# Performance work log

Measured on AMD Instinct MI355X. Metric: run time of the kernel, lower is better.

## Reference

```python
import jax, jax.numpy as jnp
import numpy as np

B, T, N, D, H = 16, 128, 64, 256, 512

def _xavier(key, shape):
    fan_in, fan_out = shape[0], shape[1]
    limit = float(np.sqrt(6.0 / (fan_in + fan_out)))
    return jax.random.uniform(key, shape, jnp.float32, -limit, limit)

def setup_inputs() -> dict:
    key = jax.random.key(0)
    ks = jax.random.split(key, 12)
    inp = {
        'x1': jax.random.normal(ks[0], (B, T, N, D), jnp.float32),
        'x2': jax.random.normal(ks[1], (B, T, N, D), jnp.float32),
        'Wq1': _xavier(ks[2], (D, H)),
        'Wk1': _xavier(ks[3], (D, H)),
        'Wv1': _xavier(ks[4], (D, H)),
        'Wq2': _xavier(ks[5], (D, H)),
        'Wk2': _xavier(ks[6], (D, H)),
        'Wv2': _xavier(ks[7], (D, H)),
        'W1': _xavier(ks[8], (2 * H, H)),
        'b1': jnp.zeros((H,), jnp.float32),
        'W2': _xavier(ks[9], (H, H)),
        'b2': jnp.zeros((H,), jnp.float32),
    }
    return inp

def reference(x1, x2, Wq1, Wk1, Wv1, Wq2, Wk2, Wv2, W1, b1, W2, b2):
    scale = x1.shape[-1] ** (-0.5)  # scales by in_dim, as in the original
    q1 = jnp.einsum('btnd,dh->btnh', x1, Wq1) * scale
    k1 = jnp.einsum('btnd,dh->btnh', x1, Wk1)
    v1 = jnp.einsum('btnd,dh->btnh', x1, Wv1)
    q2 = jnp.einsum('btnd,dh->btnh', x2, Wq2) * scale
    k2 = jnp.einsum('btnd,dh->btnh', x2, Wk2)
    v2 = jnp.einsum('btnd,dh->btnh', x2, Wv2)
    # cross attention 1: q1 attends over k2, aggregates v1 (faithful to source)
    s1 = jnp.einsum('btnh,btmh->btnm', q1, k2)
    a1 = jnp.einsum('btnm,btmh->btnh', jax.nn.softmax(s1, axis=-1), v1)
    # cross attention 2: q2 attends over k1, aggregates v2
    s2 = jnp.einsum('btnh,btmh->btnm', q2, k1)
    a2 = jnp.einsum('btnm,btmh->btnh', jax.nn.softmax(s2, axis=-1), v2)
    x = jnp.concatenate([a1, a2], axis=-1)  # [B,T,N,2H]
    h = jax.nn.relu(jnp.einsum('btnf,fh->btnh', x, W1) + b1)
    return jnp.einsum('btnh,hk->btnk', h, W2) + b2
```

## Files before the change

kernel.cpp:

```cpp
#include <hip/hip_runtime.h>
#include <stdint.h>

#define NB 64
#define DD 256
#define HH 512
#define NGROUP 2048

typedef __attribute__((ext_vector_type(8))) _Float16 half8;
typedef __attribute__((ext_vector_type(4))) _Float16 half4;
typedef __attribute__((ext_vector_type(4))) float f32x4;

__device__ __forceinline__ half8 ld8(const _Float16* p) {
    return *reinterpret_cast<const half8*>(p);
}

__device__ __forceinline__ int fragidx(int R, int K, int NKS) {
    return (((R >> 4) * NKS + (K >> 5)) * 64 + (((K >> 3) & 3) * 16 + (R & 15))) * 8 + (K & 7);
}

__global__ void prep_all(const float* __restrict__ Wq1, const float* __restrict__ Wk1,
                         const float* __restrict__ Wv1, const float* __restrict__ Wq2,
                         const float* __restrict__ Wk2, const float* __restrict__ Wv2,
                         const float* __restrict__ W1, const float* __restrict__ W2,
                         _Float16* __restrict__ Gf1, _Float16* __restrict__ Gf2,
                         _Float16* __restrict__ UTf, _Float16* __restrict__ W2Tf,
                         float scale) {
    const int b = blockIdx.x, t = threadIdx.x;
    if (b < 512) {
        const float* A = (b < 256) ? Wq1 : Wq2;
        const float* Bm = (b < 256) ? Wk2 : Wk1;
        _Float16* G = (b < 256) ? Gf1 : Gf2;
        const int d = b & 255, e = t;
        const float4* qa = reinterpret_cast<const float4*>(A + d * HH);
        const float4* ka = reinterpret_cast<const float4*>(Bm + e * HH);
        float s = 0.f;
        #pragma unroll 8
        for (int j = 0; j < HH / 4; ++j) {
            float4 a = qa[j], bb = ka[j];
            s += a.x * bb.x + a.y * bb.y + a.z * bb.z + a.w * bb.w;
        }
        G[fragidx(d, e, 8)] = (_Float16)(s * scale);
    } else if (b < 1536) {
        const int half = (b - 512) >> 9;
        const int o = (b - 512) & 511;
        const float* Wv = half ? Wv2 : Wv1;
        const float* W1p = W1 + half * HH * HH;
        const int d = t;
        const float4* va = reinterpret_cast<const float4*>(Wv + d * HH);
        float s = 0.f;
        #pragma unroll 4
        for (int j4 = 0; j4 < HH / 4; ++j4) {
            float4 a = va[j4];
            const int j = j4 * 4;
            s += a.x * W1p[(j + 0) * HH + o];
            s += a.y * W1p[(j + 1) * HH + o];
            s += a.z * W1p[(j + 2) * HH + o];
            s += a.w * W1p[(j + 3) * HH + o];
        }
        UTf[fragidx(o, half * 256 + d, 16)] = (_Float16)s;
    } else {
        __shared__ float tile[32][33];
        const int bi = b - 1536;
        const int bk = (bi & 15) * 32;
        const int bh = (bi >> 4) * 32;
        const int tx = t & 31, ty = t >> 5;
        #pragma unroll
        for (int i = 0; i < 32; i += 8)
            tile[ty + i][tx] = W2[(bh + ty + i) * HH + bk + tx];
        __syncthreads();
        #pragma unroll
        for (int i = 0; i < 32; i += 8) {
            const int R = bk + ty + i;
            const int K = bh + tx;
            W2Tf[fragidx(R, K, 16)] = (_Float16)tile[tx][ty + i];
        }
    }
}

#define ABASE 65536
#define PBASE 131072

__device__ __forceinline__ int axX(int side, int row, int ec) {
    return side * 32768 + row * 512 +
           ((2 * ec) ^ ((row & 7) << 4) ^ (((row >> 3) & 1) << 7));
}
__device__ __forceinline__ int axA(int side, int row, int ec) {
    return ABASE + side * 32768 + row * 512 +
           ((2 * ec) ^ ((row & 7) << 4) ^ (((row >> 3) & 1) << 7));
}
__device__ __forceinline__ int axXT(int side, int row, int ec) {
    return ABASE + side * 32768 + row * 128 + ((2 * ec) ^ ((row & 7) << 4));
}
__device__ __forceinline__ int axH(int row, int ec) {
    return ABASE + row * 1024 +
           ((2 * ec) ^ ((row & 7) << 4) ^ (((row >> 3) & 1) << 7));
}
__device__ __forceinline__ int axP(int side, int row, int ec) {
    return PBASE + side * 8192 + row * 128 + ((2 * ec) ^ ((row & 7) << 4));
}

__global__ __launch_bounds__(1024, 4)
void fused_kernel(const float* __restrict__ x1g, const float* __restrict__ x2g,
                  const _Float16* __restrict__ Gf1, const _Float16* __restrict__ Gf2,
                  const _Float16* __restrict__ UTf, const _Float16* __restrict__ W2Tf,
                  const float* __restrict__ b1, const float* __restrict__ b2,
                  float* __restrict__ out) {
    __shared__ __align__(16) char lds[147456];

    const int tid = threadIdx.x;
    const int lane = tid & 63;
    const int w = tid >> 6;
    const int c = lane & 15;
    const int kg = lane >> 4;
    const int s = w >> 3;
    const int ws = w & 7;
    const size_t g = blockIdx.x;
    const f32x4 z = {0.f, 0.f, 0.f, 0.f};

    {
        const float* xs0 = x1g + g * (NB * DD);
        const float* xs1 = x2g + g * (NB * DD);
        #pragma unroll
        for (int it = 0; it < 4; ++it) {
            const int row = 4 * w + it;
            float4 a = reinterpret_cast<const float4*>(xs0 + row * DD)[lane];
            float4 b = reinterpret_cast<const float4*>(xs1 + row * DD)[lane];
            half4 ha, hb;
            ha[0] = (_Float16)a.x; ha[1] = (_Float16)a.y; ha[2] = (_Float16)a.z; ha[3] = (_Float16)a.w;
            hb[0] = (_Float16)b.x; hb[1] = (_Float16)b.y; hb[2] = (_Float16)b.z; hb[3] = (_Float16)b.w;
            *reinterpret_cast<half4*>(lds + axX(0, row, 4 * lane)) = ha;
            *reinterpret_cast<half4*>(lds + axX(1, row, 4 * lane)) = hb;
        }
    }
    __syncthreads();

    {
        const _Float16* Gsel = s ? Gf2 : Gf1;
        const int xo = 1 - s;
        f32x4 acc[4][2];
        #pragma unroll
        for (int i = 0; i < 4; ++i) { acc[i][0] = z; acc[i][1] = z; }
        #pragma unroll
        for (int ks = 0; ks < 8; ++ks) {
            half8 af[4];
            #pragma unroll
            for (int i = 0; i < 4; ++i)
                af[i] = *reinterpret_cast<const half8*>(lds + axX(xo, 16 * i + c, 32 * ks + 8 * kg));
            #pragma unroll
            for (int ct = 0; ct < 2; ++ct) {
                half8 bf = ld8(Gsel + (((2 * ws + ct) * 8 + ks) * 64 + lane) * 8);
                #pragma unroll
                for (int i = 0; i < 4; ++i)
                    acc[i][ct] = __builtin_amdgcn_mfma_f32_16x16x32_f16(af[i], bf, acc[i][ct], 0, 0, 0);
            }
        }
        #pragma unroll
        for (int i = 0; i < 4; ++i)
            #pragma unroll
            for (int ct = 0; ct < 2; ++ct)
                #pragma unroll
                for (int r = 0; r < 4; ++r)
                    *reinterpret_cast<_Float16*>(lds + axA(s, 16 * i + 4 * kg + r, 32 * ws + 16 * ct + c)) = (_Float16)acc[i][ct][r];
    }
    __syncthreads();

    if ((w & 4) == 0) {
        const int wa = w & 3;
        f32x4 Sacc[4] = {z, z, z, z};
        #pragma unroll
        for (int ks = 0; ks < 8; ++ks) {
            half8 af = *reinterpret_cast<const half8*>(lds + axX(s, 16 * wa + c, 32 * ks + 8 * kg));
            #pragma unroll
            for (int j = 0; j < 4; ++j) {
                half8 bfr = *reinterpret_cast<const half8*>(lds + axA(s, 16 * j + c, 32 * ks + 8 * kg));
                Sacc[j] = __builtin_amdgcn_mfma_f32_16x16x32_f16(af, bfr, Sacc[j], 0, 0, 0);
            }
        }
        #pragma unroll
        for (int r = 0; r < 4; ++r) {
            float m0 = fmaxf(fmaxf(Sacc[0][r], Sacc[1][r]), fmaxf(Sacc[2][r], Sacc[3][r]));
            m0 = fmaxf(m0, __shfl_xor(m0, 1));
            m0 = fmaxf(m0, __shfl_xor(m0, 2));
            m0 = fmaxf(m0, __shfl_xor(m0, 4));
            m0 = fmaxf(m0, __shfl_xor(m0, 8));
            float e0 = __expf(Sacc[0][r] - m0);
            float e1 = __expf(Sacc[1][r] - m0);
            float e2 = __expf(Sacc[2][r] - m0);
            float e3 = __expf(Sacc[3][r] - m0);
            float s0 = e0 + e1 + e2 + e3;
            s0 += __shfl_xor(s0, 1);
            s0 += __shfl_xor(s0, 2);
            s0 += __shfl_xor(s0, 4);
            s0 += __shfl_xor(s0, 8);
            const float inv = 1.f / s0;
            const int row = 16 * wa + 4 * kg + r;
            *reinterpret_cast<_Float16*>(lds + axP(s, row, 16 * 0 + c)) = (_Float16)(e0 * inv);
            *reinterpret_cast<_Float16*>(lds + axP(s, row, 16 * 1 + c)) = (_Float16)(e1 * inv);
            *reinterpret_cast<_Float16*>(lds + axP(s, row, 16 * 2 + c)) = (_Float16)(e2 * inv);
            *reinterpret_cast<_Float16*>(lds + axP(s, row, 16 * 3 + c)) = (_Float16)(e3 * inv);
        }
    }
    __syncthreads();

    {
        #pragma unroll
        for (int jj = 0; jj < 4; ++jj) {
            half8 v = *reinterpret_cast<const half8*>(lds + axX(s, lane, 32 * ws + 8 * jj));
            #pragma unroll
            for (int e = 0; e < 8; ++e)
                *reinterpret_cast<_Float16*>(lds + axXT(s, 32 * ws + 8 * jj + e, lane)) = v[e];
        }
    }
    __syncthreads();

    {
        half8 paf[4][2];
        #pragma unroll
        for (int i = 0; i < 4; ++i)
            #pragma unroll
            for (int ksp = 0; ksp < 2; ++ksp)
                paf[i][ksp] = *reinterpret_cast<const half8*>(lds + axP(s, 16 * i + c, 32 * ksp + 8 * kg));
        #pragma unroll
        for (int dt = 0; dt < 2; ++dt) {
            half8 bfr0 = *reinterpret_cast<const half8*>(lds + axXT(s, 32 * ws + 16 * dt + c, 8 * kg));
            half8 bfr1 = *reinterpret_cast<const half8*>(lds + axXT(s, 32 * ws + 16 * dt + c, 32 + 8 * kg));
            #pragma unroll
            for (int i = 0; i < 4; ++i) {
                f32x4 acc = z;
                acc = __builtin_amdgcn_mfma_f32_16x16x32_f16(paf[i][0], bfr0, acc, 0, 0, 0);
                acc = __builtin_amdgcn_mfma_f32_16x16x32_f16(paf[i][1], bfr1, acc, 0, 0, 0);
                #pragma unroll
                for (int r = 0; r < 4; ++r)
                    *reinterpret_cast<_Float16*>(lds + axX(s, 16 * i + 4 * kg + r, 32 * ws + 16 * dt + c)) = (_Float16)acc[r];
            }
        }
    }
    __syncthreads();

    {
        f32x4 acc[4][2];
        #pragma unroll
        for (int i = 0; i < 4; ++i) { acc[i][0] = z; acc[i][1] = z; }
        #pragma unroll
        for (int ks = 0; ks < 16; ++ks) {
            const int side = ks >> 3, kk = ks & 7;
            half8 af[4];
            #pragma unroll
            for (int i = 0; i < 4; ++i)
                af[i] = *reinterpret_cast<const half8*>(lds + axX(side, 16 * i + c, 32 * kk + 8 * kg));
            #pragma unroll
            for (int ct = 0; ct < 2; ++ct) {
                half8 bf = ld8(UTf + (((2 * w + ct) * 16 + ks) * 64 + lane) * 8);
                #pragma unroll
                for (int i = 0; i < 4; ++i)
                    acc[i][ct] = __builtin_amdgcn_mfma_f32_16x16x32_f16(af[i], bf, acc[i][ct], 0, 0, 0);
            }
        }
        #pragma unroll
        for (int ct = 0; ct < 2; ++ct) {
            const float bb = b1[32 * w + 16 * ct + c];
            #pragma unroll
            for (int i = 0; i < 4; ++i)
                #pragma unroll
                for (int r = 0; r < 4; ++r)
                    *reinterpret_cast<_Float16*>(lds + axH(16 * i + 4 * kg + r, 32 * w + 16 * ct + c)) =
                        (_Float16)fmaxf(acc[i][ct][r] + bb, 0.f);
        }
    }
    __syncthreads();

    {
        f32x4 oacc[2][4];
        #pragma unroll
        for (int i = 0; i < 2; ++i)
            #pragma unroll
            for (int nj = 0; nj < 4; ++nj) oacc[i][nj] = z;
        #pragma unroll
        for (int ks = 0; ks < 16; ++ks) {
            half8 bfr2[4];
            #pragma unroll
            for (int nj = 0; nj < 4; ++nj)
                bfr2[nj] = *reinterpret_cast<const half8*>(lds + axH(16 * nj + c, 32 * ks + 8 * kg));
            #pragma unroll
            for (int i = 0; i < 2; ++i) {
                half8 af2 = ld8(W2Tf + (((2 * w + i) * 16 + ks) * 64 + lane) * 8);
                #pragma unroll
                for (int nj = 0; nj < 4; ++nj)
                    oacc[i][nj] = __builtin_amdgcn_mfma_f32_16x16x32_f16(af2, bfr2[nj], oacc[i][nj], 0, 0, 0);
            }
        }
        float* og = out + g * (size_t)(NB * HH);
        #pragma unroll
        for (int i = 0; i < 2; ++i) {
            const int ocol0 = 32 * w + 16 * i + 4 * kg;
            const float4 b2v = *reinterpret_cast<const float4*>(b2 + ocol0);
            #pragma unroll
            for (int nj = 0; nj < 4; ++nj) {
                float4 res;
                res.x = oacc[i][nj][0] + b2v.x;
                res.y = oacc[i][nj][1] + b2v.y;
                res.z = oacc[i][nj][2] + b2v.z;
                res.w = oacc[i][nj][3] + b2v.w;
                *reinterpret_cast<float4*>(og + (size_t)(16 * nj + c) * HH + ocol0) = res;
            }
        }
    }
}


extern "C" void kernel_launch(void* const* d_in, const int* in_sizes, int n_in,
                              void* d_out, int out_size, void* d_ws, size_t ws_size,
                              hipStream_t stream) {
    (void)in_sizes; (void)n_in; (void)out_size; (void)ws_size;
    const float* x1  = (const float*)d_in[0];
    const float* x2  = (const float*)d_in[1];
    const float* Wq1 = (const float*)d_in[2];
    const float* Wk1 = (const float*)d_in[3];
    const float* Wv1 = (const float*)d_in[4];
    const float* Wq2 = (const float*)d_in[5];
    const float* Wk2 = (const float*)d_in[6];
    const float* Wv2 = (const float*)d_in[7];
    const float* W1  = (const float*)d_in[8];
    const float* b1  = (const float*)d_in[9];
    const float* W2  = (const float*)d_in[10];
    const float* b2  = (const float*)d_in[11];
    float* out = (float*)d_out;

    char* ws = (char*)d_ws;
    _Float16* Gf1  = (_Float16*)(ws + 0);
    _Float16* Gf2  = (_Float16*)(ws + 131072);
    _Float16* UTf  = (_Float16*)(ws + 262144);
    _Float16* W2Tf = (_Float16*)(ws + 786432);

    const float scale = 0.0625f;

    prep_all<<<1792, 256, 0, stream>>>(Wq1, Wk1, Wv1, Wq2, Wk2, Wv2, W1, W2,
                                       Gf1, Gf2, UTf, W2Tf, scale);
    fused_kernel<<<NGROUP, 1024, 0, stream>>>(x1, x2, Gf1, Gf2, UTf, W2Tf, b1, b2, out);
}
```

Before: 443.7 us.

## Restructure fused kernel to 512 threads with smaller LDS footprint and chunked stages

Halves the block size to 512 threads and cuts shared memory from 144KB to 80KB by chunking the score, transpose/PV and MLP stages into column slices that reuse a small rotating LDS region, doing the transpose and PV outputs in place over the x buffers. The first projection now uses 32x32x16 MFMA with a new fragment layout for G. The aim is to fit more blocks per CU (LDS-limited before). In exchange there are many more __syncthreads per block and each wave does more serial work.

```diff
diff --git a/kernel.cpp b/kernel.cpp
--- a/kernel.cpp
+++ b/kernel.cpp
@@ -9,6 +9,7 @@
 typedef __attribute__((ext_vector_type(8))) _Float16 half8;
 typedef __attribute__((ext_vector_type(4))) _Float16 half4;
 typedef __attribute__((ext_vector_type(4))) float f32x4;
+typedef __attribute__((ext_vector_type(16))) float f32x16;
 
 __device__ __forceinline__ half8 ld8(const _Float16* p) {
     return *reinterpret_cast<const half8*>(p);
@@ -16,6 +17,9 @@
 
 __device__ __forceinline__ int fragidx(int R, int K, int NKS) {
     return (((R >> 4) * NKS + (K >> 5)) * 64 + (((K >> 3) & 3) * 16 + (R & 15))) * 8 + (K & 7);
+}
+__device__ __forceinline__ int fragidx32(int R, int K, int NK16) {
+    return (((R >> 5) * NK16 + (K >> 4)) * 64 + (((K >> 3) & 1) * 32 + (R & 31))) * 8 + (K & 7);
 }
 
 __global__ void prep_all(const float* __restrict__ Wq1, const float* __restrict__ Wk1,
@@ -39,7 +43,7 @@
             float4 a = qa[j], bb = ka[j];
             s += a.x * bb.x + a.y * bb.y + a.z * bb.z + a.w * bb.w;
         }
-        G[fragidx(d, e, 8)] = (_Float16)(s * scale);
+        G[fragidx32(d, e, 16)] = (_Float16)(s * scale);
     } else if (b < 1536) {
         const int half = (b - 512) >> 9;
         const int o = (b - 512) & 511;
@@ -77,52 +81,42 @@
     }
 }
 
-#define ABASE 65536
-#define PBASE 131072
+#define RBASE 65536
 
 __device__ __forceinline__ int axX(int side, int row, int ec) {
     return side * 32768 + row * 512 +
            ((2 * ec) ^ ((row & 7) << 4) ^ (((row >> 3) & 1) << 7));
 }
-__device__ __forceinline__ int axA(int side, int row, int ec) {
-    return ABASE + side * 32768 + row * 512 +
-           ((2 * ec) ^ ((row & 7) << 4) ^ (((row >> 3) & 1) << 7));
-}
-__device__ __forceinline__ int axXT(int side, int row, int ec) {
-    return ABASE + side * 32768 + row * 128 + ((2 * ec) ^ ((row & 7) << 4));
-}
-__device__ __forceinline__ int axH(int row, int ec) {
-    return ABASE + row * 1024 +
-           ((2 * ec) ^ ((row & 7) << 4) ^ (((row >> 3) & 1) << 7));
-}
-__device__ __forceinline__ int axP(int side, int row, int ec) {
-    return PBASE + side * 8192 + row * 128 + ((2 * ec) ^ ((row & 7) << 4));
-}
-
-__global__ __launch_bounds__(1024, 4)
+__device__ __forceinline__ int axR(int slot, int row, int ec) {
+    return RBASE + slot * 8192 + row * 128 + ((2 * ec) ^ ((row & 7) << 4));
+}
+
+__global__ __launch_bounds__(512, 4)
 void fused_kernel(const float* __restrict__ x1g, const float* __restrict__ x2g,
                   const _Float16* __restrict__ Gf1, const _Float16* __restrict__ Gf2,
                   const _Float16* __restrict__ UTf, const _Float16* __restrict__ W2Tf,
                   const float* __restrict__ b1, const float* __restrict__ b2,
                   float* __restrict__ out) {
-    __shared__ __align__(16) char lds[147456];
+    __shared__ __align__(16) char lds[81920];
 
     const int tid = threadIdx.x;
     const int lane = tid & 63;
     const int w = tid >> 6;
     const int c = lane & 15;
     const int kg = lane >> 4;
-    const int s = w >> 3;
-    const int ws = w & 7;
+    const int c5 = lane & 31;
+    const int kg2 = lane >> 5;
     const size_t g = blockIdx.x;
     const f32x4 z = {0.f, 0.f, 0.f, 0.f};
+    const f32x16 z16 = {0.f,0.f,0.f,0.f,0.f,0.f,0.f,0.f,0.f,0.f,0.f,0.f,0.f,0.f,0.f,0.f};
+    #define ROWF(r) ((((r) & 3) + 8 * ((r) >> 2)) + 4 * kg2)
 
     {
         const float* xs0 = x1g + g * (NB * DD);
         const float* xs1 = x2g + g * (NB * DD);
         #pragma unroll
-        for (int it = 0; it < 4; ++it) {
-            const int row = 4 * w + it;
+        for (int it = 0; it < 8; ++it) {
+            const int row = 8 * w + it;
             float4 a = reinterpret_cast<const float4*>(xs0 + row * DD)[lane];
             float4 b = reinterpret_cast<const float4*>(xs1 + row * DD)[lane];
             half4 ha, hb;
@@ -134,48 +128,40 @@
     }
     __syncthreads();
 
+    f32x4 Sacc[4] = {z, z, z, z};
+    const int sW = w >> 2;
+    const int wa = w & 3;
     {
-        const _Float16* Gsel = s ? Gf2 : Gf1;
-        const int xo = 1 - s;
-        f32x4 acc[4][2];
-        #pragma unroll
-        for (int i = 0; i < 4; ++i) { acc[i][0] = z; acc[i][1] = z; }
-        #pragma unroll
-        for (int ks = 0; ks < 8; ++ks) {
-            half8 af[4];
-            #pragma unroll
-            for (int i = 0; i < 4; ++i)
-                af[i] = *reinterpret_cast<const half8*>(lds + axX(xo, 16 * i + c, 32 * ks + 8 * kg));
-            #pragma unroll
-            for (int ct = 0; ct < 2; ++ct) {
-                half8 bf = ld8(Gsel + (((2 * ws + ct) * 8 + ks) * 64 + lane) * 8);
+        const int rb = (w >> 1) & 1, cb = w & 1;
+        const _Float16* Gsel = sW ? Gf2 : Gf1;
+        const int xo = 1 - sW;
+        #pragma unroll 1
+        for (int ci = 0; ci < 4; ++ci) {
+            f32x16 acc = z16;
+            #pragma unroll
+            for (int ks = 0; ks < 16; ++ks) {
+                half8 af = *reinterpret_cast<const half8*>(lds + axX(xo, 32 * rb + c5, 16 * ks + 8 * kg2));
+                half8 bf = ld8(Gsel + (((2 * ci + cb) * 16 + ks) * 64 + lane) * 8);
+                acc = __builtin_amdgcn_mfma_f32_32x32x16_f16(af, bf, acc, 0, 0, 0);
+            }
+            #pragma unroll
+            for (int r = 0; r < 16; ++r)
+                *reinterpret_cast<_Float16*>(lds + axR(sW, 32 * rb + ROWF(r), 32 * cb + c5)) = (_Float16)acc[r];
+            __syncthreads();
+            #pragma unroll
+            for (int ks = 0; ks < 2; ++ks) {
+                half8 af = *reinterpret_cast<const half8*>(lds + axX(sW, 16 * wa + c, 64 * ci + 32 * ks + 8 * kg));
                 #pragma unroll
-                for (int i = 0; i < 4; ++i)
-                    acc[i][ct] = __builtin_amdgcn_mfma_f32_16x16x32_f16(af[i], bf, acc[i][ct], 0, 0, 0);
-            }
-        }
-        #pragma unroll
-        for (int i = 0; i < 4; ++i)
-            #pragma unroll
-            for (int ct = 0; ct < 2; ++ct)
-                #pragma unroll
-                for (int r = 0; r < 4; ++r)
-                    *reinterpret_cast<_Float16*>(lds + axA(s, 16 * i + 4 * kg + r, 32 * ws + 16 * ct + c)) = (_Float16)acc[i][ct][r];
-    }
-    __syncthreads();
-
-    if ((w & 4) == 0) {
-        const int wa = w & 3;
-        f32x4 Sacc[4] = {z, z, z, z};
-        #pragma unroll
-        for (int ks = 0; ks < 8; ++ks) {
-            half8 af = *reinterpret_cast<const half8*>(lds + axX(s, 16 * wa + c, 32 * ks + 8 * kg));
-            #pragma unroll
-            for (int j = 0; j < 4; ++j) {
-                half8 bfr = *reinterpret_cast<const half8*>(lds + axA(s, 16 * j + c, 32 * ks + 8 * kg));
-                Sacc[j] = __builtin_amdgcn_mfma_f32_16x16x32_f16(af, bfr, Sacc[j], 0, 0, 0);
-            }
-        }
+                for (int j = 0; j < 4; ++j) {
+                    half8 bfr = *reinterpret_cast<const half8*>(lds + axR(sW, 16 * j + c, 32 * ks + 8 * kg));
+                    Sacc[j] = __builtin_amdgcn_mfma_f32_16x16x32_f16(af, bfr, Sacc[j], 0, 0, 0);
+                }
+            }
+            __syncthreads();
+        }
+    }
+
+    {
         #pragma unroll
         for (int r = 0; r < 4; ++r) {
             float m0 = fmaxf(fmaxf(Sacc[0][r], Sacc[1][r]), fmaxf(Sacc[2][r], Sacc[3][r]));
@@ -194,21 +180,10 @@
             s0 += __shfl_xor(s0, 8);
             const float inv = 1.f / s0;
             const int row = 16 * wa + 4 * kg + r;
-            *reinterpret_cast<_Float16*>(lds + axP(s, row, 16 * 0 + c)) = (_Float16)(e0 * inv);
-            *reinterpret_cast<_Float16*>(lds + axP(s, row, 16 * 1 + c)) = (_Float16)(e1 * inv);
-            *reinterpret_cast<_Float16*>(lds + axP(s, row, 16 * 2 + c)) = (_Float16)(e2 * inv);
-            *reinterpret_cast<_Float16*>(lds + axP(s, row, 16 * 3 + c)) = (_Float16)(e3 * inv);
-        }
-    }
-    __syncthreads();
-
-    {
-        #pragma unroll
-        for (int jj = 0; jj < 4; ++jj) {
-            half8 v = *reinterpret_cast<const half8*>(lds + axX(s, lane, 32 * ws + 8 * jj));
-            #pragma unroll
-            for (int e = 0; e < 8; ++e)
-                *reinterpret_cast<_Float16*>(lds + axXT(s, 32 * ws + 8 * jj + e, lane)) = v[e];
+            *reinterpret_cast<_Float16*>(lds + axR(sW, row, 16 * 0 + c)) = (_Float16)(e0 * inv);
+            *reinterpret_cast<_Float16*>(lds + axR(sW, row, 16 * 1 + c)) = (_Float16)(e1 * inv);
+            *reinterpret_cast<_Float16*>(lds + axR(sW, row, 16 * 2 + c)) = (_Float16)(e2 * inv);
+            *reinterpret_cast<_Float16*>(lds + axR(sW, row, 16 * 3 + c)) = (_Float16)(e3 * inv);
         }
     }
     __syncthreads();
@@ -219,92 +194,104 @@
         for (int i = 0; i < 4; ++i)
             #pragma unroll
             for (int ksp = 0; ksp < 2; ++ksp)
-                paf[i][ksp] = *reinterpret_cast<const half8*>(lds + axP(s, 16 * i + c, 32 * ksp + 8 * kg));
-        #pragma unroll
-        for (int dt = 0; dt < 2; ++dt) {
-            half8 bfr0 = *reinterpret_cast<const half8*>(lds + axXT(s, 32 * ws + 16 * dt + c, 8 * kg));
-            half8 bfr1 = *reinterpret_cast<const half8*>(lds + axXT(s, 32 * ws + 16 * dt + c, 32 + 8 * kg));
+                paf[i][ksp] = *reinterpret_cast<const half8*>(lds + axR(sW, 16 * i + c, 32 * ksp + 8 * kg));
+
+        const int tside = tid >> 8;
+        const int tloc = tid & 255;
+        const int tm = tloc >> 2, tq = tloc & 3;
+        #pragma unroll 1
+        for (int ci = 0; ci < 4; ++ci) {
+            half8 v0 = *reinterpret_cast<const half8*>(lds + axX(tside, tm, 64 * ci + 16 * tq));
+            half8 v1 = *reinterpret_cast<const half8*>(lds + axX(tside, tm, 64 * ci + 16 * tq + 8));
+            __syncthreads();
+            #pragma unroll
+            for (int e = 0; e < 8; ++e) {
+                *reinterpret_cast<_Float16*>(lds + axX(tside, 16 * tq + e,     64 * ci + tm)) = v0[e];
+                *reinterpret_cast<_Float16*>(lds + axX(tside, 16 * tq + 8 + e, 64 * ci + tm)) = v1[e];
+            }
+            __syncthreads();
+            half8 bfr0 = *reinterpret_cast<const half8*>(lds + axX(sW, 16 * wa + c, 64 * ci + 8 * kg));
+            half8 bfr1 = *reinterpret_cast<const half8*>(lds + axX(sW, 16 * wa + c, 64 * ci + 32 + 8 * kg));
+            f32x4 ga[4];
             #pragma unroll
             for (int i = 0; i < 4; ++i) {
                 f32x4 acc = z;
                 acc = __builtin_amdgcn_mfma_f32_16x16x32_f16(paf[i][0], bfr0, acc, 0, 0, 0);
                 acc = __builtin_amdgcn_mfma_f32_16x16x32_f16(paf[i][1], bfr1, acc, 0, 0, 0);
-                #pragma unroll
-                for (int r = 0; r < 4; ++r)
-                    *reinterpret_cast<_Float16*>(lds + axX(s, 16 * i + 4 * kg + r, 32 * ws + 16 * dt + c)) = (_Float16)acc[r];
-            }
-        }
-    }
-    __syncthreads();
-
-    {
-        f32x4 acc[4][2];
-        #pragma unroll
-        for (int i = 0; i < 4; ++i) { acc[i][0] = z; acc[i][1] = z; }
-        #pragma unroll
-        for (int ks = 0; ks < 16; ++ks) {
-            const int side = ks >> 3, kk = ks & 7;
-            half8 af[4];
-            #pragma unroll
-            for (int i = 0; i < 4; ++i)
-                af[i] = *reinterpret_cast<const half8*>(lds + axX(side, 16 * i + c, 32 * kk + 8 * kg));
-            #pragma unroll
-            for (int ct = 0; ct < 2; ++ct) {
-                half8 bf = ld8(UTf + (((2 * w + ct) * 16 + ks) * 64 + lane) * 8);
-                #pragma unroll
-                for (int i = 0; i < 4; ++i)
-                    acc[i][ct] = __builtin_amdgcn_mfma_f32_16x16x32_f16(af[i], bf, acc[i][ct], 0, 0, 0);
-            }
-        }
-        #pragma unroll
-        for (int ct = 0; ct < 2; ++ct) {
-            const float bb = b1[32 * w + 16 * ct + c];
+                ga[i] = acc;
+            }
+            __syncthreads();
             #pragma unroll
             for (int i = 0; i < 4; ++i)
                 #pragma unroll
                 for (int r = 0; r < 4; ++r)
-                    *reinterpret_cast<_Float16*>(lds + axH(16 * i + 4 * kg + r, 32 * w + 16 * ct + c)) =
-                        (_Float16)fmaxf(acc[i][ct][r] + bb, 0.f);
+                    *reinterpret_cast<_Float16*>(lds + axX(sW, 16 * i + 4 * kg + r, 64 * ci + 16 * wa + c)) = (_Float16)ga[i][r];
         }
     }
     __syncthreads();
 
-    {
-        f32x4 oacc[2][4];
-        #pragma unroll
-        for (int i = 0; i < 2; ++i)
-            #pragma unroll
-            for (int nj = 0; nj < 4; ++nj) oacc[i][nj] = z;
+    f32x4 oacc[4][4];
+    #pragma unroll
+    for (int i = 0; i < 4; ++i)
+        #pragma unroll
+        for (int j = 0; j < 4; ++j) oacc[i][j] = z;
+
+    const int ct2 = w >> 1;
+    const int rh = w & 1;
+    #pragma unroll 1
+    for (int q = 0; q < 8; ++q) {
+        const int buf = q & 1;
+        f32x4 hacc[2] = {z, z};
         #pragma unroll
         for (int ks = 0; ks < 16; ++ks) {
+            const int side = ks >> 3, kk = ks & 7;
+            half8 bf = ld8(UTf + (((4 * q + ct2) * 16 + ks) * 64 + lane) * 8);
+            #pragma unroll
+            for (int i2 = 0; i2 < 2; ++i2) {
+                half8 af = *reinterpret_cast<const half8*>(lds + axX(side, 16 * (2 * rh + i2) + c, 32 * kk + 8 * kg));
+                hacc[i2] = __builtin_amdgcn_mfma_f32_16x16x32_f16(af, bf, hacc[i2], 0, 0, 0);
+            }
+        }
+        const float bb = b1[64 * q + 16 * ct2 + c];
+        #pragma unroll
+        for (int i2 = 0; i2 < 2; ++i2)
+            #pragma unroll
+            for (int r = 0; r < 4; ++r)
+                *reinterpret_cast<_Float16*>(lds + axR(buf, 16 * (2 * rh + i2) + 4 * kg + r, 16 * ct2 + c)) =
+                    (_Float16)fmaxf(hacc[i2][r] + bb, 0.f);
+        __syncthreads();
+        #pragma unroll
+        for (int ks = 0; ks < 2; ++ks) {
             half8 bfr2[4];
             #pragma unroll
             for (int nj = 0; nj < 4; ++nj)
-                bfr2[nj] = *reinterpret_cast<const half8*>(lds + axH(16 * nj + c, 32 * ks + 8 * kg));
-            #pragma unroll
-            for (int i = 0; i < 2; ++i) {
-                half8 af2 = ld8(W2Tf + (((2 * w + i) * 16 + ks) * 64 + lane) * 8);
+                bfr2[nj] = *reinterpret_cast<const half8*>(lds + axR(buf, 16 * nj + c, 32 * ks + 8 * kg));
+            #pragma unroll
+            for (int i = 0; i < 4; ++i) {
+                half8 af2 = ld8(W2Tf + (((4 * w + i) * 16 + 2 * q + ks) * 64 + lane) * 8);
                 #pragma unroll
                 for (int nj = 0; nj < 4; ++nj)
                     oacc[i][nj] = __builtin_amdgcn_mfma_f32_16x16x32_f16(af2, bfr2[nj], oacc[i][nj], 0, 0, 0);
             }
         }
-        float* og = out + g * (size_t)(NB * HH);
-        #pragma unroll
-        for (int i = 0; i < 2; ++i) {
-            const int ocol0 = 32 * w + 16 * i + 4 * kg;
-            const float4 b2v = *reinterpret_cast<const float4*>(b2 + ocol0);
-            #pragma unroll
-            for (int nj = 0; nj < 4; ++nj) {
-                float4 res;
-                res.x = oacc[i][nj][0] + b2v.x;
-                res.y = oacc[i][nj][1] + b2v.y;
-                res.z = oacc[i][nj][2] + b2v.z;
-                res.w = oacc[i][nj][3] + b2v.w;
-                *reinterpret_cast<float4*>(og + (size_t)(16 * nj + c) * HH + ocol0) = res;
-            }
-        }
-    }
+    }
+
+    float* og = out + g * (size_t)(NB * HH);
+    #pragma unroll
+    for (int i = 0; i < 4; ++i) {
+        const int ocol0 = 64 * w + 16 * i + 4 * kg;
+        const float4 b2v = *reinterpret_cast<const float4*>(b2 + ocol0);
+        #pragma unroll
+        for (int nj = 0; nj < 4; ++nj) {
+            float4 res;
+            res.x = oacc[i][nj][0] + b2v.x;
+            res.y = oacc[i][nj][1] + b2v.y;
+            res.z = oacc[i][nj][2] + b2v.z;
+            res.w = oacc[i][nj][3] + b2v.w;
+            *reinterpret_cast<float4*>(og + (size_t)(16 * nj + c) * HH + ocol0) = res;
+        }
+    }
+    #undef ROWF
 }
 
 
@@ -336,5 +323,5 @@
 
     prep_all<<<1792, 256, 0, stream>>>(Wq1, Wk1, Wv1, Wq2, Wk2, Wv2, W1, W2,
                                        Gf1, Gf2, UTf, W2Tf, scale);
-    fused_kernel<<<NGROUP, 1024, 0, stream>>>(x1, x2, Gf1, Gf2, UTf, W2Tf, b1, b2, out);
-}
+    fused_kernel<<<NGROUP, 512, 0, stream>>>(x1, x2, Gf1, Gf2, UTf, W2Tf, b1, b2, out);
+}
```

After: 508.2 us. 14.5% more time.
